# Optimization experiments

Measured on AMD Instinct MI355X. Metric: run time of the kernel, lower is better.

The kernel has to match this reference:

```python
import jax, jax.numpy as jnp
import numpy as np

K_PERIODS = 6


def setup_inputs() -> dict:
    key = jax.random.key(0)
    x = jax.random.normal(key, (16, 2048, 128), dtype=jnp.float32)
    return {"x": x}


def reference(x):
    # x: [B, T, N] -> out: [B, K, Pmax, N].
    # Pmax is data-dependent in the torch original (max selected period); here we
    # use the static upper bound Pmax = T so shapes are jit-static. Columns
    # p >= P_row are zero, matching the original's zero padding.
    B, T, N = x.shape
    BN = B * N
    seqs = jnp.transpose(x, (0, 2, 1)).reshape(BN, T)  # [BN, T]

    # --- top-k nonzero frequencies by spectral energy ---
    spec = jnp.fft.rfft(seqs, axis=-1)
    mag2 = spec.real ** 2 + spec.imag ** 2
    mag2 = mag2.at[:, 0].set(0.0)  # kill DC bin
    k = min(K_PERIODS, mag2.shape[-1] - 1)
    _, kidx = jax.lax.top_k(mag2, k)          # [BN, K]
    kidx = jnp.maximum(kidx, 1)

    # --- per-(row, freq) period geometry ---
    P = jnp.maximum(T // kidx, 1)             # [BN, K] period length
    cycles = jnp.maximum(T // P, 1)           # [BN, K] number of full cycles
    take = cycles * P
    base = jnp.maximum(T - take, 0)           # [BN, K] start offset

    # --- fold-and-average via scatter-add (no [BN,K,Cmax,Pmax] blowup) ---
    # element at time t >= base maps to phase p = (t - base) % P, averaged over cycles
    t = jnp.arange(T, dtype=jnp.int32)
    rel = t[None, None, :] - base[:, :, None]          # [BN, K, T]
    valid = rel >= 0
    p = jnp.where(valid, rel % P[:, :, None], 0)       # phase index in [0, P)
    vals = jnp.where(valid, seqs[:, None, :], 0.0)     # [BN, K, T]

    row = jnp.arange(BN * k, dtype=jnp.int32).reshape(BN, k, 1)
    seg_ids = row * T + p                               # flat segment id
    sums = jax.ops.segment_sum(vals.reshape(-1), seg_ids.reshape(-1),
                               num_segments=BN * k * T)
    seg = sums.reshape(BN, k, T) / cycles[:, :, None].astype(vals.dtype)

    out = seg.reshape(B, N, k, T).transpose(0, 2, 3, 1)  # [B, K, Pmax=T, N]
    return out
```

## Files before the change

kernel.cpp:

```cpp
#include <hip/hip_runtime.h>
#include <stdint.h>

#define TB   256
#define TLEN 2048
#define NB   16
#define NCH  128
#define BN   (NB*NCH)
#define KP   6

typedef unsigned long long u64;

__device__ inline float2 cmul(float2 a, float2 b) {
  return make_float2(a.x * b.x - a.y * b.y, a.x * b.y + a.y * b.x);
}
__device__ inline float2 cadd(float2 a, float2 b) { return make_float2(a.x + b.x, a.y + b.y); }
__device__ inline float2 csub(float2 a, float2 b) { return make_float2(a.x - b.x, a.y - b.y); }
__device__ inline float2 cmni(float2 a) { return make_float2(a.y, -a.x); }

__global__ __launch_bounds__(256) void k_prep(const float* __restrict__ x,
                                              float* __restrict__ seqs,
                                              float4* __restrict__ out4, int n4) {
  int bid = blockIdx.x;
  if (bid < 1024) {
    __shared__ float tile[64][65];
    int tb = bid & 31, nb = (bid >> 5) & 1, b = bid >> 6;
    int t0 = tb * 64, n0 = nb * 64;
    int tx = threadIdx.x & 63, ty = threadIdx.x >> 6;
#pragma unroll
    for (int tt = ty; tt < 64; tt += 4)
      tile[tt][tx] = x[(size_t)(b * TLEN + t0 + tt) * NCH + n0 + tx];
    __syncthreads();
#pragma unroll
    for (int nn = ty; nn < 64; nn += 4)
      seqs[(size_t)(b * NCH + n0 + nn) * TLEN + t0 + tx] = tile[tx][nn];
  } else {
    int i = (bid - 1024) * 256 + threadIdx.x;
    if (i < n4) out4[i] = make_float4(0.f, 0.f, 0.f, 0.f);
  }
}

#define PAD(o) ((o) + ((o) >> 4))
#define C2 0.70710678118654752f

__global__ __launch_bounds__(256) void k_fft_fold(const float* __restrict__ seqs,
                                                  float* __restrict__ out) {
  __shared__ __align__(16) float2 bufA[2176];
  __shared__ __align__(16) float2 bufB[2176];
  __shared__ float2 tw[256];
  __shared__ u64 wmax[4];
  __shared__ int4 prm[2][KP];
  int tid = threadIdx.x, lane = tid & 63, wv = tid >> 6;
  int r0 = blockIdx.x * 2;
  const float* row0 = seqs + (size_t)r0 * TLEN;

#pragma unroll
  for (int k = 0; k < 8; k++) {
    int t = tid + k * TB;
    bufA[PAD(t)] = make_float2(row0[t], row0[t + TLEN]);
  }
  {
    float sn, cs;
    sincosf((-6.283185307179586f / 2048.f) * (float)tid, &sn, &cs);
    tw[tid & 255] = make_float2(cs, sn);
  }

  float2* xb = bufA;
  float2* yb = bufB;
#pragma unroll
  for (int stage = 0; stage < 3; stage++) {
    int s = (stage == 0) ? 1 : (stage == 1) ? 8 : 64;
    __syncthreads();
    int i = tid;
    int q = i & (s - 1);
    int cb = i - q;
    float2 A0 = xb[PAD(i)],        A1 = xb[PAD(i + 256)],
           A2 = xb[PAD(i + 512)],  A3 = xb[PAD(i + 768)],
           A4 = xb[PAD(i + 1024)], A5 = xb[PAD(i + 1280)],
           A6 = xb[PAD(i + 1536)], A7 = xb[PAD(i + 1792)];
    float2 s02 = cadd(A0, A4), d02 = csub(A0, A4);
    float2 s13 = cadd(A2, A6), d13 = csub(A2, A6);
    float2 E0 = cadd(s02, s13), E1 = cadd(d02, cmni(d13));
    float2 E2 = csub(s02, s13), E3 = csub(d02, cmni(d13));
    float2 t02 = cadd(A1, A5), e02 = csub(A1, A5);
    float2 t13 = cadd(A3, A7), e13 = csub(A3, A7);
    float2 O0 = cadd(t02, t13), O1 = cadd(e02, cmni(e13));
    float2 O2 = csub(t02, t13), O3 = csub(e02, cmni(e13));
    float2 T0 = O0;
    float2 T1 = make_float2(C2 * (O1.x + O1.y), C2 * (O1.y - O1.x));
    float2 T2 = cmni(O2);
    float2 T3 = make_float2(C2 * (O3.y - O3.x), -C2 * (O3.x + O3.y));
    float2 B0 = cadd(E0, T0), B4 = csub(E0, T0);
    float2 B1 = cadd(E1, T1), B5 = csub(E1, T1);
    float2 B2 = cadd(E2, T2), B6 = csub(E2, T2);
    float2 B3 = cadd(E3, T3), B7 = csub(E3, T3);
    float2 w1 = tw[cb];
    float2 w2 = cmul(w1, w1);
    float2 w3 = cmul(w2, w1);
    float2 w4 = cmul(w2, w2);
    float2 w5 = cmul(w4, w1);
    float2 w6 = cmul(w4, w2);
    float2 w7 = cmul(w4, w3);
    int o = q + 8 * cb;
    yb[PAD(o)]         = B0;
    yb[PAD(o + s)]     = cmul(w1, B1);
    yb[PAD(o + 2 * s)] = cmul(w2, B2);
    yb[PAD(o + 3 * s)] = cmul(w3, B3);
    yb[PAD(o + 4 * s)] = cmul(w4, B4);
    yb[PAD(o + 5 * s)] = cmul(w5, B5);
    yb[PAD(o + 6 * s)] = cmul(w6, B6);
    yb[PAD(o + 7 * s)] = cmul(w7, B7);
    float2* tp = xb; xb = yb; yb = tp;
  }
  __syncthreads();
#pragma unroll
  for (int ii = 0; ii < 2; ii++) {
    int i = tid + ii * TB;
    float2 a0 = xb[PAD(i)], a1 = xb[PAD(i + 512)];
    float2 a2 = xb[PAD(i + 1024)], a3 = xb[PAD(i + 1536)];
    float2 S02 = cadd(a0, a2), D02 = csub(a0, a2);
    float2 S13 = cadd(a1, a3), D13 = csub(a1, a3);
    yb[PAD(i)]        = cadd(S02, S13);
    yb[PAD(i + 512)]  = cadd(D02, cmni(D13));
    yb[PAD(i + 1024)] = csub(S02, S13);
    yb[PAD(i + 1536)] = csub(D02, cmni(D13));
  }
  __syncthreads();

  const float2* Z = bufA;
  u64* keys = (u64*)bufB;
  for (int i = tid; i < 1024; i += TB) {
    int kb = i + 1;
    float2 zk = Z[PAD(kb)];
    float2 zc = Z[PAD(2048 - kb)];
    float ax = zk.x + zc.x, ay = zk.y - zc.y;
    float bx = zk.x - zc.x, by = zk.y + zc.y;
    float m2a = ax * ax + ay * ay;
    float m2b = bx * bx + by * by;
    keys[i]        = ((u64)__float_as_uint(m2a) << 32) | (unsigned)(0xFFFFFFFFu - (unsigned)kb);
    keys[1024 + i] = ((u64)__float_as_uint(m2b) << 32) | (unsigned)(0xFFFFFFFFu - (unsigned)kb);
  }
  __syncthreads();

  float* srows = (float*)bufA;
  {
    const float4* s4 = (const float4*)row0;
    float4* r4 = (float4*)srows;
    for (int i = tid; i < 1024; i += TB) r4[i] = s4[i];
  }

  int rw2 = wv >> 1;
  u64* kb2 = keys + rw2 * 1024;
  int t2 = tid & 127;
  for (int r = 0; r < KP; r++) {
    u64 best = 0ull;
    for (int i = t2; i < 1024; i += 128) {
      u64 v = kb2[i];
      best = v > best ? v : best;
    }
    for (int off = 32; off > 0; off >>= 1) {
      u64 o = __shfl_down(best, off);
      best = o > best ? o : best;
    }
    if (lane == 0) wmax[wv] = best;
    __syncthreads();
    if (t2 == 0) {
      u64 b0 = wmax[rw2 * 2], b1 = wmax[rw2 * 2 + 1];
      best = b0 > b1 ? b0 : b1;
      int bin = (int)(0xFFFFFFFFu - (unsigned)(best & 0xFFFFFFFFull));
      if (bin < 1 || bin > 1024) bin = 1;
      kb2[bin - 1] = 0ull;
      int P = TLEN / bin;
      int cyc = TLEN / P;
      int base = TLEN - cyc * P;
      prm[rw2][r] = make_int4(P, base, cyc, 0);
    }
    __syncthreads();
  }

  for (int task = wv; task < 2 * KP; task += 4) {
    int rw = task & 1, k = task >> 1;
    int4 pr = prm[rw][k];
    int P = pr.x, base = pr.y, cyc = pr.z;
    float inv = 1.0f / (float)cyc;
    const float* srow = srows + rw * TLEN;
    int row = r0 + rw, b = row >> 7, n = row & 127;
    float* dst = out + (size_t)(b * KP + k) * TLEN * NCH + n;

    if (P >= 64) {
      for (int p = lane; p < P; p += 64) {
        const float* sp = srow + base + p;
        float s = 0.f;
        for (int c = 0; c < cyc; c++) s += sp[c * P];
        dst[(size_t)p * NCH] = s * inv;
      }
    } else {
      int wc = 64 / P, u = wc * P, ci = lane / P;
      float v = 0.f;
      if (lane < u) {
        for (int c0 = 0; c0 < cyc; c0 += wc) {
          int c = c0 + ci;
          if (c < cyc) v += srow[base + c0 * P + lane];
        }
      }
      for (int s = P; s < u; s <<= 1) {
        float o = __shfl_down(v, s);
        if (lane + s < u) v += o;
      }
      if (lane < P) dst[(size_t)lane * NCH] = v * inv;
    }
  }
}

extern "C" void kernel_launch(void* const* d_in, const int* in_sizes, int n_in,
                              void* d_out, int out_size, void* d_ws, size_t ws_size,
                              hipStream_t stream) {
  const float* x = (const float*)d_in[0];
  float* out = (float*)d_out;
  float* seqs = (float*)d_ws;

  int n4 = out_size / 4;
  int fill_blocks = (n4 + 255) / 256;
  k_prep<<<1024 + fill_blocks, 256, 0, stream>>>(x, seqs, (float4*)out, n4);
  k_fft_fold<<<BN / 2, 256, 0, stream>>>(seqs, out);
}
```

Before: 145.1 us.

## Fuse transpose into FFT kernel and replace zero-fill with masked expand pass

Removes the separate transpose/zero-fill kernel. The FFT kernel now reads x directly as float2 pairs of adjacent channels and keeps the raw rows in shared memory. Folded results go to a contiguous per-row workspace along with the period lengths. A new expand kernel writes the final [B,K,T,N] output once as float4, emitting zeros for phases beyond each row's period. This avoids a full-output memset followed by strided scattered writes, but adds an extra pass over a workspace the size of the output and more shared memory per block.

```diff
diff --git a/kernel.cpp b/kernel.cpp
--- a/kernel.cpp
+++ b/kernel.cpp
@@ -17,117 +17,116 @@
 __device__ inline float2 csub(float2 a, float2 b) { return make_float2(a.x - b.x, a.y - b.y); }
 __device__ inline float2 cmni(float2 a) { return make_float2(a.y, -a.x); }
 
-__global__ __launch_bounds__(256) void k_prep(const float* __restrict__ x,
-                                              float* __restrict__ seqs,
-                                              float4* __restrict__ out4, int n4) {
-  int bid = blockIdx.x;
-  if (bid < 1024) {
-    __shared__ float tile[64][65];
-    int tb = bid & 31, nb = (bid >> 5) & 1, b = bid >> 6;
-    int t0 = tb * 64, n0 = nb * 64;
-    int tx = threadIdx.x & 63, ty = threadIdx.x >> 6;
-#pragma unroll
-    for (int tt = ty; tt < 64; tt += 4)
-      tile[tt][tx] = x[(size_t)(b * TLEN + t0 + tt) * NCH + n0 + tx];
-    __syncthreads();
-#pragma unroll
-    for (int nn = ty; nn < 64; nn += 4)
-      seqs[(size_t)(b * NCH + n0 + nn) * TLEN + t0 + tx] = tile[tx][nn];
-  } else {
-    int i = (bid - 1024) * 256 + threadIdx.x;
-    if (i < n4) out4[i] = make_float4(0.f, 0.f, 0.f, 0.f);
-  }
-}
-
 #define PAD(o) ((o) + ((o) >> 4))
 #define C2 0.70710678118654752f
 
-__global__ __launch_bounds__(256) void k_fft_fold(const float* __restrict__ seqs,
-                                                  float* __restrict__ out) {
+__device__ inline void radix8(const float2 A[8], float2 w1, float2 B[8]) {
+  float2 s02 = cadd(A[0], A[4]), d02 = csub(A[0], A[4]);
+  float2 s13 = cadd(A[2], A[6]), d13 = csub(A[2], A[6]);
+  float2 E0 = cadd(s02, s13), E1 = cadd(d02, cmni(d13));
+  float2 E2 = csub(s02, s13), E3 = csub(d02, cmni(d13));
+  float2 t02 = cadd(A[1], A[5]), e02 = csub(A[1], A[5]);
+  float2 t13 = cadd(A[3], A[7]), e13 = csub(A[3], A[7]);
+  float2 O0 = cadd(t02, t13), O1 = cadd(e02, cmni(e13));
+  float2 O2 = csub(t02, t13), O3 = csub(e02, cmni(e13));
+  float2 T0 = O0;
+  float2 T1 = make_float2(C2 * (O1.x + O1.y), C2 * (O1.y - O1.x));
+  float2 T2 = cmni(O2);
+  float2 T3 = make_float2(C2 * (O3.y - O3.x), -C2 * (O3.x + O3.y));
+  float2 b0 = cadd(E0, T0), b4 = csub(E0, T0);
+  float2 b1 = cadd(E1, T1), b5 = csub(E1, T1);
+  float2 b2 = cadd(E2, T2), b6 = csub(E2, T2);
+  float2 b3 = cadd(E3, T3), b7 = csub(E3, T3);
+  float2 w2 = cmul(w1, w1);
+  float2 w3 = cmul(w2, w1);
+  float2 w4 = cmul(w2, w2);
+  float2 w5 = cmul(w4, w1);
+  float2 w6 = cmul(w4, w2);
+  float2 w7 = cmul(w4, w3);
+  B[0] = b0;
+  B[1] = cmul(w1, b1);
+  B[2] = cmul(w2, b2);
+  B[3] = cmul(w3, b3);
+  B[4] = cmul(w4, b4);
+  B[5] = cmul(w5, b5);
+  B[6] = cmul(w6, b6);
+  B[7] = cmul(w7, b7);
+}
+
+__global__ __launch_bounds__(256) void k_fft_fold(const float* __restrict__ x,
+                                                  float* __restrict__ seg,
+                                                  int* __restrict__ Pg) {
   __shared__ __align__(16) float2 bufA[2176];
   __shared__ __align__(16) float2 bufB[2176];
+  __shared__ float sraw[2][TLEN];
   __shared__ float2 tw[256];
   __shared__ u64 wmax[4];
   __shared__ int4 prm[2][KP];
   int tid = threadIdx.x, lane = tid & 63, wv = tid >> 6;
   int r0 = blockIdx.x * 2;
-  const float* row0 = seqs + (size_t)r0 * TLEN;
-
-#pragma unroll
-  for (int k = 0; k < 8; k++) {
-    int t = tid + k * TB;
-    bufA[PAD(t)] = make_float2(row0[t], row0[t + TLEN]);
+  int b = r0 >> 7, n0 = r0 & 127;
+
+  const float2* x2 = (const float2*)x;
+  size_t xoff = (size_t)b * TLEN * 64 + (n0 >> 1);
+#pragma unroll
+  for (int kk = 0; kk < 8; kk++) {
+    int t = tid + kk * TB;
+    float2 v = x2[xoff + (size_t)t * 64];
+    sraw[0][t] = v.x;
+    sraw[1][t] = v.y;
   }
   {
     float sn, cs;
     sincosf((-6.283185307179586f / 2048.f) * (float)tid, &sn, &cs);
-    tw[tid & 255] = make_float2(cs, sn);
-  }
-
-  float2* xb = bufA;
-  float2* yb = bufB;
-#pragma unroll
-  for (int stage = 0; stage < 3; stage++) {
-    int s = (stage == 0) ? 1 : (stage == 1) ? 8 : 64;
+    tw[tid] = make_float2(cs, sn);
+  }
+  __syncthreads();
+
+  {
+    int i = tid;
+    float2 A[8], B[8];
+#pragma unroll
+    for (int j = 0; j < 8; j++)
+      A[j] = make_float2(sraw[0][i + j * 256], sraw[1][i + j * 256]);
+    radix8(A, tw[i], B);
+    int o = 8 * i;
+#pragma unroll
+    for (int j = 0; j < 8; j++) bufA[PAD(o + j)] = B[j];
+  }
+#pragma unroll
+  for (int stage = 0; stage < 2; stage++) {
+    int s = stage == 0 ? 8 : 64;
+    float2* xb = stage == 0 ? bufA : bufB;
+    float2* yb = stage == 0 ? bufB : bufA;
     __syncthreads();
     int i = tid;
     int q = i & (s - 1);
     int cb = i - q;
-    float2 A0 = xb[PAD(i)],        A1 = xb[PAD(i + 256)],
-           A2 = xb[PAD(i + 512)],  A3 = xb[PAD(i + 768)],
-           A4 = xb[PAD(i + 1024)], A5 = xb[PAD(i + 1280)],
-           A6 = xb[PAD(i + 1536)], A7 = xb[PAD(i + 1792)];
-    float2 s02 = cadd(A0, A4), d02 = csub(A0, A4);
-    float2 s13 = cadd(A2, A6), d13 = csub(A2, A6);
-    float2 E0 = cadd(s02, s13), E1 = cadd(d02, cmni(d13));
-    float2 E2 = csub(s02, s13), E3 = csub(d02, cmni(d13));
-    float2 t02 = cadd(A1, A5), e02 = csub(A1, A5);
-    float2 t13 = cadd(A3, A7), e13 = csub(A3, A7);
-    float2 O0 = cadd(t02, t13), O1 = cadd(e02, cmni(e13));
-    float2 O2 = csub(t02, t13), O3 = csub(e02, cmni(e13));
-    float2 T0 = O0;
-    float2 T1 = make_float2(C2 * (O1.x + O1.y), C2 * (O1.y - O1.x));
-    float2 T2 = cmni(O2);
-    float2 T3 = make_float2(C2 * (O3.y - O3.x), -C2 * (O3.x + O3.y));
-    float2 B0 = cadd(E0, T0), B4 = csub(E0, T0);
-    float2 B1 = cadd(E1, T1), B5 = csub(E1, T1);
-    float2 B2 = cadd(E2, T2), B6 = csub(E2, T2);
-    float2 B3 = cadd(E3, T3), B7 = csub(E3, T3);
-    float2 w1 = tw[cb];
-    float2 w2 = cmul(w1, w1);
-    float2 w3 = cmul(w2, w1);
-    float2 w4 = cmul(w2, w2);
-    float2 w5 = cmul(w4, w1);
-    float2 w6 = cmul(w4, w2);
-    float2 w7 = cmul(w4, w3);
+    float2 A[8], B[8];
+#pragma unroll
+    for (int j = 0; j < 8; j++) A[j] = xb[PAD(i + j * 256)];
+    radix8(A, tw[cb], B);
     int o = q + 8 * cb;
-    yb[PAD(o)]         = B0;
-    yb[PAD(o + s)]     = cmul(w1, B1);
-    yb[PAD(o + 2 * s)] = cmul(w2, B2);
-    yb[PAD(o + 3 * s)] = cmul(w3, B3);
-    yb[PAD(o + 4 * s)] = cmul(w4, B4);
-    yb[PAD(o + 5 * s)] = cmul(w5, B5);
-    yb[PAD(o + 6 * s)] = cmul(w6, B6);
-    yb[PAD(o + 7 * s)] = cmul(w7, B7);
-    float2* tp = xb; xb = yb; yb = tp;
+#pragma unroll
+    for (int j = 0; j < 8; j++) yb[PAD(o + j * s)] = B[j];
   }
   __syncthreads();
 #pragma unroll
   for (int ii = 0; ii < 2; ii++) {
     int i = tid + ii * TB;
-    float2 a0 = xb[PAD(i)], a1 = xb[PAD(i + 512)];
-    float2 a2 = xb[PAD(i + 1024)], a3 = xb[PAD(i + 1536)];
+    float2 a0 = bufA[PAD(i)], a1 = bufA[PAD(i + 512)];
+    float2 a2 = bufA[PAD(i + 1024)], a3 = bufA[PAD(i + 1536)];
     float2 S02 = cadd(a0, a2), D02 = csub(a0, a2);
     float2 S13 = cadd(a1, a3), D13 = csub(a1, a3);
-    yb[PAD(i)]        = cadd(S02, S13);
-    yb[PAD(i + 512)]  = cadd(D02, cmni(D13));
-    yb[PAD(i + 1024)] = csub(S02, S13);
-    yb[PAD(i + 1536)] = csub(D02, cmni(D13));
-  }
-  __syncthreads();
-
-  const float2* Z = bufA;
-  u64* keys = (u64*)bufB;
+    bufB[PAD(i)]        = cadd(S02, S13);
+    bufB[PAD(i + 512)]  = cadd(D02, cmni(D13));
+    bufB[PAD(i + 1024)] = csub(S02, S13);
+    bufB[PAD(i + 1536)] = csub(D02, cmni(D13));
+  }
+  __syncthreads();
+
+  const float2* Z = bufB;
+  u64* keys = (u64*)bufA;
   for (int i = tid; i < 1024; i += TB) {
     int kb = i + 1;
     float2 zk = Z[PAD(kb)];
@@ -140,13 +139,6 @@
     keys[1024 + i] = ((u64)__float_as_uint(m2b) << 32) | (unsigned)(0xFFFFFFFFu - (unsigned)kb);
   }
   __syncthreads();
-
-  float* srows = (float*)bufA;
-  {
-    const float4* s4 = (const float4*)row0;
-    float4* r4 = (float4*)srows;
-    for (int i = tid; i < 1024; i += TB) r4[i] = s4[i];
-  }
 
   int rw2 = wv >> 1;
   u64* kb2 = keys + rw2 * 1024;
@@ -173,6 +165,7 @@
       int cyc = TLEN / P;
       int base = TLEN - cyc * P;
       prm[rw2][r] = make_int4(P, base, cyc, 0);
+      Pg[(r0 + rw2) * KP + r] = P;
     }
     __syncthreads();
   }
@@ -182,16 +175,15 @@
     int4 pr = prm[rw][k];
     int P = pr.x, base = pr.y, cyc = pr.z;
     float inv = 1.0f / (float)cyc;
-    const float* srow = srows + rw * TLEN;
-    int row = r0 + rw, b = row >> 7, n = row & 127;
-    float* dst = out + (size_t)(b * KP + k) * TLEN * NCH + n;
+    const float* srow = sraw[rw];
+    float* dst = seg + ((size_t)(r0 + rw) * KP + k) * TLEN;
 
     if (P >= 64) {
       for (int p = lane; p < P; p += 64) {
         const float* sp = srow + base + p;
         float s = 0.f;
         for (int c = 0; c < cyc; c++) s += sp[c * P];
-        dst[(size_t)p * NCH] = s * inv;
+        dst[p] = s * inv;
       }
     } else {
       int wc = 64 / P, u = wc * P, ci = lane / P;
@@ -206,8 +198,34 @@
         float o = __shfl_down(v, s);
         if (lane + s < u) v += o;
       }
-      if (lane < P) dst[(size_t)lane * NCH] = v * inv;
-    }
+      if (lane < P) dst[lane] = v * inv;
+    }
+  }
+}
+
+__global__ __launch_bounds__(256) void k_expand(const float* __restrict__ seg,
+                                                const int* __restrict__ Pg,
+                                                float4* __restrict__ out4) {
+  __shared__ int Parr[NCH];
+  int z = blockIdx.x;
+  int pc = z & 15, bk = z >> 4;
+  int b = bk / KP, k = bk - KP * b;
+  int tid = threadIdx.x;
+  if (tid < NCH) Parr[tid] = Pg[(b * NCH + tid) * KP + k];
+  __syncthreads();
+  int p0 = pc * 128;
+  for (int e = tid; e < 4096; e += TB) {
+    int p = p0 + (e >> 5);
+    int n4 = (e & 31) * 4;
+    float4 v = make_float4(0.f, 0.f, 0.f, 0.f);
+    float* vp = &v.x;
+#pragma unroll
+    for (int c = 0; c < 4; c++) {
+      int n = n4 + c;
+      if (p < Parr[n])
+        vp[c] = seg[((size_t)(b * NCH + n) * KP + k) * TLEN + p];
+    }
+    out4[((size_t)bk * TLEN + p) * (NCH / 4) + (e & 31)] = v;
   }
 }
 
@@ -216,10 +234,12 @@
                               hipStream_t stream) {
   const float* x = (const float*)d_in[0];
   float* out = (float*)d_out;
-  float* seqs = (float*)d_ws;
-
-  int n4 = out_size / 4;
-  int fill_blocks = (n4 + 255) / 256;
-  k_prep<<<1024 + fill_blocks, 256, 0, stream>>>(x, seqs, (float4*)out, n4);
-  k_fft_fold<<<BN / 2, 256, 0, stream>>>(seqs, out);
-}
+  char* ws = (char*)d_ws;
+
+  const size_t seg_bytes = (size_t)BN * KP * TLEN * 4;
+  float* seg = (float*)ws;
+  int* Pg = (int*)(ws + seg_bytes);
+
+  k_fft_fold<<<BN / 2, 256, 0, stream>>>(x, seg, Pg);
+  k_expand<<<NB * KP * 16, 256, 0, stream>>>(seg, Pg, (float4*)out);
+}
```

Result: slower. 164.5 us (+13.3%).

## Do top-k selection in registers per wavefront, removing block barriers

Applied to the files above, without the earlier changes.

Each of the first two wavefronts now builds the spectral-energy keys for one row in registers (16 per lane) and runs the six rounds of top-k with wave-wide xor shuffles. This replaces the shared-memory key array and the two block-wide barriers per round. Meanwhile the other two wavefronts copy the raw rows into shared memory, so the copy overlaps the selection. The cost is higher register pressure from 16 u64 keys per lane, and only half the block is busy during selection.

```diff
diff --git a/kernel.cpp b/kernel.cpp
--- a/kernel.cpp
+++ b/kernel.cpp
@@ -16,6 +16,42 @@
 __device__ inline float2 cadd(float2 a, float2 b) { return make_float2(a.x + b.x, a.y + b.y); }
 __device__ inline float2 csub(float2 a, float2 b) { return make_float2(a.x - b.x, a.y - b.y); }
 __device__ inline float2 cmni(float2 a) { return make_float2(a.y, -a.x); }
+
+#define PAD(o) ((o) + ((o) >> 4))
+#define C2 0.70710678118654752f
+
+__device__ inline void radix8(const float2 A[8], float2 w1, float2 B[8]) {
+  float2 s02 = cadd(A[0], A[4]), d02 = csub(A[0], A[4]);
+  float2 s13 = cadd(A[2], A[6]), d13 = csub(A[2], A[6]);
+  float2 E0 = cadd(s02, s13), E1 = cadd(d02, cmni(d13));
+  float2 E2 = csub(s02, s13), E3 = csub(d02, cmni(d13));
+  float2 t02 = cadd(A[1], A[5]), e02 = csub(A[1], A[5]);
+  float2 t13 = cadd(A[3], A[7]), e13 = csub(A[3], A[7]);
+  float2 O0 = cadd(t02, t13), O1 = cadd(e02, cmni(e13));
+  float2 O2 = csub(t02, t13), O3 = csub(e02, cmni(e13));
+  float2 T0 = O0;
+  float2 T1 = make_float2(C2 * (O1.x + O1.y), C2 * (O1.y - O1.x));
+  float2 T2 = cmni(O2);
+  float2 T3 = make_float2(C2 * (O3.y - O3.x), -C2 * (O3.x + O3.y));
+  float2 b0 = cadd(E0, T0), b4 = csub(E0, T0);
+  float2 b1 = cadd(E1, T1), b5 = csub(E1, T1);
+  float2 b2 = cadd(E2, T2), b6 = csub(E2, T2);
+  float2 b3 = cadd(E3, T3), b7 = csub(E3, T3);
+  float2 w2 = cmul(w1, w1);
+  float2 w3 = cmul(w2, w1);
+  float2 w4 = cmul(w2, w2);
+  float2 w5 = cmul(w4, w1);
+  float2 w6 = cmul(w4, w2);
+  float2 w7 = cmul(w4, w3);
+  B[0] = b0;
+  B[1] = cmul(w1, b1);
+  B[2] = cmul(w2, b2);
+  B[3] = cmul(w3, b3);
+  B[4] = cmul(w4, b4);
+  B[5] = cmul(w5, b5);
+  B[6] = cmul(w6, b6);
+  B[7] = cmul(w7, b7);
+}
 
 __global__ __launch_bounds__(256) void k_prep(const float* __restrict__ x,
                                               float* __restrict__ seqs,
@@ -39,23 +75,19 @@
   }
 }
 
-#define PAD(o) ((o) + ((o) >> 4))
-#define C2 0.70710678118654752f
-
 __global__ __launch_bounds__(256) void k_fft_fold(const float* __restrict__ seqs,
                                                   float* __restrict__ out) {
   __shared__ __align__(16) float2 bufA[2176];
   __shared__ __align__(16) float2 bufB[2176];
   __shared__ float2 tw[256];
-  __shared__ u64 wmax[4];
   __shared__ int4 prm[2][KP];
   int tid = threadIdx.x, lane = tid & 63, wv = tid >> 6;
   int r0 = blockIdx.x * 2;
   const float* row0 = seqs + (size_t)r0 * TLEN;
 
 #pragma unroll
-  for (int k = 0; k < 8; k++) {
-    int t = tid + k * TB;
+  for (int kk = 0; kk < 8; kk++) {
+    int t = tid + kk * TB;
     bufA[PAD(t)] = make_float2(row0[t], row0[t + TLEN]);
   }
   {
@@ -64,118 +96,86 @@
     tw[tid & 255] = make_float2(cs, sn);
   }
 
-  float2* xb = bufA;
-  float2* yb = bufB;
 #pragma unroll
   for (int stage = 0; stage < 3; stage++) {
     int s = (stage == 0) ? 1 : (stage == 1) ? 8 : 64;
+    float2* xb = (stage == 1) ? bufB : bufA;
+    float2* yb = (stage == 1) ? bufA : bufB;
     __syncthreads();
     int i = tid;
     int q = i & (s - 1);
     int cb = i - q;
-    float2 A0 = xb[PAD(i)],        A1 = xb[PAD(i + 256)],
-           A2 = xb[PAD(i + 512)],  A3 = xb[PAD(i + 768)],
-           A4 = xb[PAD(i + 1024)], A5 = xb[PAD(i + 1280)],
-           A6 = xb[PAD(i + 1536)], A7 = xb[PAD(i + 1792)];
-    float2 s02 = cadd(A0, A4), d02 = csub(A0, A4);
-    float2 s13 = cadd(A2, A6), d13 = csub(A2, A6);
-    float2 E0 = cadd(s02, s13), E1 = cadd(d02, cmni(d13));
-    float2 E2 = csub(s02, s13), E3 = csub(d02, cmni(d13));
-    float2 t02 = cadd(A1, A5), e02 = csub(A1, A5);
-    float2 t13 = cadd(A3, A7), e13 = csub(A3, A7);
-    float2 O0 = cadd(t02, t13), O1 = cadd(e02, cmni(e13));
-    float2 O2 = csub(t02, t13), O3 = csub(e02, cmni(e13));
-    float2 T0 = O0;
-    float2 T1 = make_float2(C2 * (O1.x + O1.y), C2 * (O1.y - O1.x));
-    float2 T2 = cmni(O2);
-    float2 T3 = make_float2(C2 * (O3.y - O3.x), -C2 * (O3.x + O3.y));
-    float2 B0 = cadd(E0, T0), B4 = csub(E0, T0);
-    float2 B1 = cadd(E1, T1), B5 = csub(E1, T1);
-    float2 B2 = cadd(E2, T2), B6 = csub(E2, T2);
-    float2 B3 = cadd(E3, T3), B7 = csub(E3, T3);
-    float2 w1 = tw[cb];
-    float2 w2 = cmul(w1, w1);
-    float2 w3 = cmul(w2, w1);
-    float2 w4 = cmul(w2, w2);
-    float2 w5 = cmul(w4, w1);
-    float2 w6 = cmul(w4, w2);
-    float2 w7 = cmul(w4, w3);
+    float2 A[8], B[8];
+#pragma unroll
+    for (int j = 0; j < 8; j++) A[j] = xb[PAD(i + j * 256)];
+    radix8(A, tw[cb], B);
     int o = q + 8 * cb;
-    yb[PAD(o)]         = B0;
-    yb[PAD(o + s)]     = cmul(w1, B1);
-    yb[PAD(o + 2 * s)] = cmul(w2, B2);
-    yb[PAD(o + 3 * s)] = cmul(w3, B3);
-    yb[PAD(o + 4 * s)] = cmul(w4, B4);
-    yb[PAD(o + 5 * s)] = cmul(w5, B5);
-    yb[PAD(o + 6 * s)] = cmul(w6, B6);
-    yb[PAD(o + 7 * s)] = cmul(w7, B7);
-    float2* tp = xb; xb = yb; yb = tp;
+#pragma unroll
+    for (int j = 0; j < 8; j++) yb[PAD(o + j * s)] = B[j];
   }
   __syncthreads();
 #pragma unroll
   for (int ii = 0; ii < 2; ii++) {
     int i = tid + ii * TB;
-    float2 a0 = xb[PAD(i)], a1 = xb[PAD(i + 512)];
-    float2 a2 = xb[PAD(i + 1024)], a3 = xb[PAD(i + 1536)];
+    float2 a0 = bufB[PAD(i)], a1 = bufB[PAD(i + 512)];
+    float2 a2 = bufB[PAD(i + 1024)], a3 = bufB[PAD(i + 1536)];
     float2 S02 = cadd(a0, a2), D02 = csub(a0, a2);
     float2 S13 = cadd(a1, a3), D13 = csub(a1, a3);
-    yb[PAD(i)]        = cadd(S02, S13);
-    yb[PAD(i + 512)]  = cadd(D02, cmni(D13));
-    yb[PAD(i + 1024)] = csub(S02, S13);
-    yb[PAD(i + 1536)] = csub(D02, cmni(D13));
+    bufA[PAD(i)]        = cadd(S02, S13);
+    bufA[PAD(i + 512)]  = cadd(D02, cmni(D13));
+    bufA[PAD(i + 1024)] = csub(S02, S13);
+    bufA[PAD(i + 1536)] = csub(D02, cmni(D13));
   }
   __syncthreads();
 
   const float2* Z = bufA;
-  u64* keys = (u64*)bufB;
-  for (int i = tid; i < 1024; i += TB) {
-    int kb = i + 1;
-    float2 zk = Z[PAD(kb)];
-    float2 zc = Z[PAD(2048 - kb)];
-    float ax = zk.x + zc.x, ay = zk.y - zc.y;
-    float bx = zk.x - zc.x, by = zk.y + zc.y;
-    float m2a = ax * ax + ay * ay;
-    float m2b = bx * bx + by * by;
-    keys[i]        = ((u64)__float_as_uint(m2a) << 32) | (unsigned)(0xFFFFFFFFu - (unsigned)kb);
-    keys[1024 + i] = ((u64)__float_as_uint(m2b) << 32) | (unsigned)(0xFFFFFFFFu - (unsigned)kb);
-  }
-  __syncthreads();
-
-  float* srows = (float*)bufA;
-  {
+  float* srows = (float*)bufB;
+
+  if (wv < 2) {
+    u64 kr[16];
+#pragma unroll
+    for (int j = 0; j < 16; j++) {
+      int kb = lane * 16 + j + 1;
+      float2 zk = Z[PAD(kb)];
+      float2 zc = Z[PAD(2048 - kb)];
+      float m2;
+      if (wv == 0) {
+        float ax = zk.x + zc.x, ay = zk.y - zc.y;
+        m2 = ax * ax + ay * ay;
+      } else {
+        float bx = zk.x - zc.x, by = zk.y + zc.y;
+        m2 = bx * bx + by * by;
+      }
+      kr[j] = ((u64)__float_as_uint(m2) << 32) | (unsigned)(0xFFFFFFFFu - (unsigned)kb);
+    }
+#pragma unroll 1
+    for (int r = 0; r < KP; r++) {
+      u64 m = kr[0];
+#pragma unroll
+      for (int j = 1; j < 16; j++) m = kr[j] > m ? kr[j] : m;
+#pragma unroll
+      for (int off = 1; off < 64; off <<= 1) {
+        u64 o = __shfl_xor(m, off);
+        m = o > m ? o : m;
+      }
+#pragma unroll
+      for (int j = 0; j < 16; j++)
+        if (kr[j] == m) kr[j] = 0ull;
+      if (lane == 0) {
+        int bin = (int)(0xFFFFFFFFu - (unsigned)(m & 0xFFFFFFFFull));
+        if (bin < 1 || bin > 1024) bin = 1;
+        int P = TLEN / bin;
+        int cyc = TLEN / P;
+        int base = TLEN - cyc * P;
+        prm[wv][r] = make_int4(P, base, cyc, 0);
+      }
+    }
+  } else {
     const float4* s4 = (const float4*)row0;
     float4* r4 = (float4*)srows;
-    for (int i = tid; i < 1024; i += TB) r4[i] = s4[i];
-  }
-
-  int rw2 = wv >> 1;
-  u64* kb2 = keys + rw2 * 1024;
-  int t2 = tid & 127;
-  for (int r = 0; r < KP; r++) {
-    u64 best = 0ull;
-    for (int i = t2; i < 1024; i += 128) {
-      u64 v = kb2[i];
-      best = v > best ? v : best;
-    }
-    for (int off = 32; off > 0; off >>= 1) {
-      u64 o = __shfl_down(best, off);
-      best = o > best ? o : best;
-    }
-    if (lane == 0) wmax[wv] = best;
-    __syncthreads();
-    if (t2 == 0) {
-      u64 b0 = wmax[rw2 * 2], b1 = wmax[rw2 * 2 + 1];
-      best = b0 > b1 ? b0 : b1;
-      int bin = (int)(0xFFFFFFFFu - (unsigned)(best & 0xFFFFFFFFull));
-      if (bin < 1 || bin > 1024) bin = 1;
-      kb2[bin - 1] = 0ull;
-      int P = TLEN / bin;
-      int cyc = TLEN / P;
-      int base = TLEN - cyc * P;
-      prm[rw2][r] = make_int4(P, base, cyc, 0);
-    }
-    __syncthreads();
-  }
+    for (int i = tid - 128; i < 1024; i += 128) r4[i] = s4[i];
+  }
+  __syncthreads();
 
   for (int task = wv; task < 2 * KP; task += 4) {
     int rw = task & 1, k = task >> 1;
```

New measurement: 144.2 us. Within noise of the previous version (-0.6%).

## Switch FFT to radix-4 stages with 512-thread blocks

Applied to the files above, without the earlier changes.

Replaces the three radix-8 Stockham stages plus radix-4 tail with five radix-4 stages and a radix-2 tail, running 512 threads per block instead of 256. Top-k key reduction and the row copy are spread over eight waves, and keys are held in registers before being written back into the reused buffer. This aims to raise parallelism and cut per-thread register pressure, at the cost of more LDS passes and barriers.

```diff
diff --git a/kernel.cpp b/kernel.cpp
--- a/kernel.cpp
+++ b/kernel.cpp
@@ -2,6 +2,7 @@
 #include <stdint.h>
 
 #define TB   256
+#define FT   512
 #define TLEN 2048
 #define NB   16
 #define NCH  128
@@ -16,6 +17,8 @@
 __device__ inline float2 cadd(float2 a, float2 b) { return make_float2(a.x + b.x, a.y + b.y); }
 __device__ inline float2 csub(float2 a, float2 b) { return make_float2(a.x - b.x, a.y - b.y); }
 __device__ inline float2 cmni(float2 a) { return make_float2(a.y, -a.x); }
+
+#define PAD(o) ((o) + ((o) >> 4))
 
 __global__ __launch_bounds__(256) void k_prep(const float* __restrict__ x,
                                               float* __restrict__ seqs,
@@ -39,122 +42,106 @@
   }
 }
 
-#define PAD(o) ((o) + ((o) >> 4))
-#define C2 0.70710678118654752f
-
-__global__ __launch_bounds__(256) void k_fft_fold(const float* __restrict__ seqs,
-                                                  float* __restrict__ out) {
+__global__ __launch_bounds__(FT, 8) void k_fft_fold(const float* __restrict__ seqs,
+                                                    float* __restrict__ out) {
   __shared__ __align__(16) float2 bufA[2176];
   __shared__ __align__(16) float2 bufB[2176];
-  __shared__ float2 tw[256];
-  __shared__ u64 wmax[4];
+  __shared__ float2 tw[512];
+  __shared__ u64 wmax[8];
   __shared__ int4 prm[2][KP];
   int tid = threadIdx.x, lane = tid & 63, wv = tid >> 6;
   int r0 = blockIdx.x * 2;
   const float* row0 = seqs + (size_t)r0 * TLEN;
 
 #pragma unroll
-  for (int k = 0; k < 8; k++) {
-    int t = tid + k * TB;
+  for (int kk = 0; kk < 4; kk++) {
+    int t = tid + kk * FT;
     bufA[PAD(t)] = make_float2(row0[t], row0[t + TLEN]);
   }
   {
     float sn, cs;
     sincosf((-6.283185307179586f / 2048.f) * (float)tid, &sn, &cs);
-    tw[tid & 255] = make_float2(cs, sn);
+    tw[tid & 511] = make_float2(cs, sn);
   }
 
   float2* xb = bufA;
   float2* yb = bufB;
 #pragma unroll
-  for (int stage = 0; stage < 3; stage++) {
-    int s = (stage == 0) ? 1 : (stage == 1) ? 8 : 64;
+  for (int st2 = 0; st2 < 10; st2 += 2) {
+    int s = 1 << st2;
     __syncthreads();
     int i = tid;
     int q = i & (s - 1);
     int cb = i - q;
-    float2 A0 = xb[PAD(i)],        A1 = xb[PAD(i + 256)],
-           A2 = xb[PAD(i + 512)],  A3 = xb[PAD(i + 768)],
-           A4 = xb[PAD(i + 1024)], A5 = xb[PAD(i + 1280)],
-           A6 = xb[PAD(i + 1536)], A7 = xb[PAD(i + 1792)];
-    float2 s02 = cadd(A0, A4), d02 = csub(A0, A4);
-    float2 s13 = cadd(A2, A6), d13 = csub(A2, A6);
-    float2 E0 = cadd(s02, s13), E1 = cadd(d02, cmni(d13));
-    float2 E2 = csub(s02, s13), E3 = csub(d02, cmni(d13));
-    float2 t02 = cadd(A1, A5), e02 = csub(A1, A5);
-    float2 t13 = cadd(A3, A7), e13 = csub(A3, A7);
-    float2 O0 = cadd(t02, t13), O1 = cadd(e02, cmni(e13));
-    float2 O2 = csub(t02, t13), O3 = csub(e02, cmni(e13));
-    float2 T0 = O0;
-    float2 T1 = make_float2(C2 * (O1.x + O1.y), C2 * (O1.y - O1.x));
-    float2 T2 = cmni(O2);
-    float2 T3 = make_float2(C2 * (O3.y - O3.x), -C2 * (O3.x + O3.y));
-    float2 B0 = cadd(E0, T0), B4 = csub(E0, T0);
-    float2 B1 = cadd(E1, T1), B5 = csub(E1, T1);
-    float2 B2 = cadd(E2, T2), B6 = csub(E2, T2);
-    float2 B3 = cadd(E3, T3), B7 = csub(E3, T3);
+    float2 A0 = xb[PAD(i)];
+    float2 A1 = xb[PAD(i + 512)];
+    float2 A2 = xb[PAD(i + 1024)];
+    float2 A3 = xb[PAD(i + 1536)];
+    float2 S02 = cadd(A0, A2), D02 = csub(A0, A2);
+    float2 S13 = cadd(A1, A3), D13 = csub(A1, A3);
+    float2 b0 = cadd(S02, S13);
+    float2 b1 = cadd(D02, cmni(D13));
+    float2 b2 = csub(S02, S13);
+    float2 b3 = csub(D02, cmni(D13));
     float2 w1 = tw[cb];
     float2 w2 = cmul(w1, w1);
-    float2 w3 = cmul(w2, w1);
-    float2 w4 = cmul(w2, w2);
-    float2 w5 = cmul(w4, w1);
-    float2 w6 = cmul(w4, w2);
-    float2 w7 = cmul(w4, w3);
-    int o = q + 8 * cb;
-    yb[PAD(o)]         = B0;
-    yb[PAD(o + s)]     = cmul(w1, B1);
-    yb[PAD(o + 2 * s)] = cmul(w2, B2);
-    yb[PAD(o + 3 * s)] = cmul(w3, B3);
-    yb[PAD(o + 4 * s)] = cmul(w4, B4);
-    yb[PAD(o + 5 * s)] = cmul(w5, B5);
-    yb[PAD(o + 6 * s)] = cmul(w6, B6);
-    yb[PAD(o + 7 * s)] = cmul(w7, B7);
-    float2* tp = xb; xb = yb; yb = tp;
+    float2 w3 = cmul(w1, w2);
+    int o = q + 4 * cb;
+    yb[PAD(o)]         = b0;
+    yb[PAD(o + s)]     = cmul(w1, b1);
+    yb[PAD(o + 2 * s)] = cmul(w2, b2);
+    yb[PAD(o + 3 * s)] = cmul(w3, b3);
+    float2* t2 = xb; xb = yb; yb = t2;
   }
   __syncthreads();
 #pragma unroll
   for (int ii = 0; ii < 2; ii++) {
-    int i = tid + ii * TB;
-    float2 a0 = xb[PAD(i)], a1 = xb[PAD(i + 512)];
-    float2 a2 = xb[PAD(i + 1024)], a3 = xb[PAD(i + 1536)];
-    float2 S02 = cadd(a0, a2), D02 = csub(a0, a2);
-    float2 S13 = cadd(a1, a3), D13 = csub(a1, a3);
-    yb[PAD(i)]        = cadd(S02, S13);
-    yb[PAD(i + 512)]  = cadd(D02, cmni(D13));
-    yb[PAD(i + 1024)] = csub(S02, S13);
-    yb[PAD(i + 1536)] = csub(D02, cmni(D13));
-  }
-  __syncthreads();
-
-  const float2* Z = bufA;
-  u64* keys = (u64*)bufB;
-  for (int i = tid; i < 1024; i += TB) {
+    int i = tid + ii * FT;
+    float2 a = bufB[PAD(i)];
+    float2 b = bufB[PAD(i + 1024)];
+    bufA[PAD(i)]        = cadd(a, b);
+    bufA[PAD(i + 1024)] = csub(a, b);
+  }
+  __syncthreads();
+
+  u64 kra[2], krb[2];
+#pragma unroll
+  for (int ii = 0; ii < 2; ii++) {
+    int i = tid + ii * FT;
     int kb = i + 1;
-    float2 zk = Z[PAD(kb)];
-    float2 zc = Z[PAD(2048 - kb)];
+    float2 zk = bufA[PAD(kb)];
+    float2 zc = bufA[PAD(2048 - kb)];
     float ax = zk.x + zc.x, ay = zk.y - zc.y;
     float bx = zk.x - zc.x, by = zk.y + zc.y;
     float m2a = ax * ax + ay * ay;
     float m2b = bx * bx + by * by;
-    keys[i]        = ((u64)__float_as_uint(m2a) << 32) | (unsigned)(0xFFFFFFFFu - (unsigned)kb);
-    keys[1024 + i] = ((u64)__float_as_uint(m2b) << 32) | (unsigned)(0xFFFFFFFFu - (unsigned)kb);
-  }
-  __syncthreads();
-
-  float* srows = (float*)bufA;
+    kra[ii] = ((u64)__float_as_uint(m2a) << 32) | (unsigned)(0xFFFFFFFFu - (unsigned)kb);
+    krb[ii] = ((u64)__float_as_uint(m2b) << 32) | (unsigned)(0xFFFFFFFFu - (unsigned)kb);
+  }
+  __syncthreads();
+  u64* keys = (u64*)bufA;
+#pragma unroll
+  for (int ii = 0; ii < 2; ii++) {
+    int i = tid + ii * FT;
+    keys[i] = kra[ii];
+    keys[1024 + i] = krb[ii];
+  }
   {
     const float4* s4 = (const float4*)row0;
-    float4* r4 = (float4*)srows;
-    for (int i = tid; i < 1024; i += TB) r4[i] = s4[i];
-  }
-
-  int rw2 = wv >> 1;
+    float4* r4 = (float4*)bufB;
+#pragma unroll
+    for (int ii = 0; ii < 2; ii++) r4[tid + ii * FT] = s4[tid + ii * FT];
+  }
+  __syncthreads();
+
+  int rw2 = wv >> 2;
   u64* kb2 = keys + rw2 * 1024;
-  int t2 = tid & 127;
+  int t2 = tid & 255;
   for (int r = 0; r < KP; r++) {
     u64 best = 0ull;
-    for (int i = t2; i < 1024; i += 128) {
-      u64 v = kb2[i];
+#pragma unroll
+    for (int j = 0; j < 4; j++) {
+      u64 v = kb2[t2 + j * 256];
       best = v > best ? v : best;
     }
     for (int off = 32; off > 0; off >>= 1) {
@@ -164,8 +151,12 @@
     if (lane == 0) wmax[wv] = best;
     __syncthreads();
     if (t2 == 0) {
-      u64 b0 = wmax[rw2 * 2], b1 = wmax[rw2 * 2 + 1];
-      best = b0 > b1 ? b0 : b1;
+      best = wmax[rw2 * 4];
+#pragma unroll
+      for (int w = 1; w < 4; w++) {
+        u64 v = wmax[rw2 * 4 + w];
+        best = v > best ? v : best;
+      }
       int bin = (int)(0xFFFFFFFFu - (unsigned)(best & 0xFFFFFFFFull));
       if (bin < 1 || bin > 1024) bin = 1;
       kb2[bin - 1] = 0ull;
@@ -177,7 +168,8 @@
     __syncthreads();
   }
 
-  for (int task = wv; task < 2 * KP; task += 4) {
+  float* srows = (float*)bufB;
+  for (int task = wv; task < 2 * KP; task += 8) {
     int rw = task & 1, k = task >> 1;
     int4 pr = prm[rw][k];
     int P = pr.x, base = pr.y, cyc = pr.z;
@@ -221,5 +213,5 @@
   int n4 = out_size / 4;
   int fill_blocks = (n4 + 255) / 256;
   k_prep<<<1024 + fill_blocks, 256, 0, stream>>>(x, seqs, (float4*)out, n4);
-  k_fft_fold<<<BN / 2, 256, 0, stream>>>(seqs, out);
-}
+  k_fft_fold<<<BN / 2, FT, 0, stream>>>(seqs, out);
+}
```

After: 146.0 us. No clear change (+0.6%).
